# Performance work log

Hardware: AMD Instinct MI355X
Metric: run time of the kernel (lower is better)

The kernel has to match this reference:

```python
import jax, jax.numpy as jnp
import numpy as np

NEG_INF = -1e30
D_MODEL = 128


def setup_inputs() -> dict:
    key = jax.random.key(0)
    k1, k2, k3 = jax.random.split(key, 3)
    B, D, Lc, Lq = 64, D_MODEL, 1024, 256
    C = jax.random.normal(k1, (B, D, Lc), dtype=jnp.float32)
    Q = jax.random.normal(k2, (B, D, Lq), dtype=jnp.float32)
    cmask = jnp.ones((B, Lc), dtype=jnp.float32)
    qmask = jnp.ones((B, Lq), dtype=jnp.float32)
    lim = (1.0 / D) ** 0.5
    w = jax.random.uniform(k3, (3 * D,), dtype=jnp.float32, minval=-lim, maxval=lim)
    return {"C": C, "Q": Q, "cmask": cmask, "qmask": qmask, "w": w}


def reference(C, Q, cmask, qmask, w):
    # C: (B, D, Lc), Q: (B, D, Lq), w: (3D,)
    D = C.shape[1]
    Ct = jnp.swapaxes(C, 1, 2)  # (B, Lc, D)
    Qt = jnp.swapaxes(Q, 1, 2)  # (B, Lq, D)
    w1, w2, w3 = w[:D], w[D:2 * D], w[2 * D:]
    # Decomposed trilinear similarity: equivalent to cat([Ct,Qt,Ct*Qt]) @ w
    S = (jnp.einsum('bld,d->bl', Ct, w1)[:, :, None]
         + jnp.einsum('bmd,d->bm', Qt, w2)[:, None, :]
         + jnp.einsum('bld,bmd->blm', Ct * w3, Qt))  # (B, Lc, Lq)
    qm = qmask[:, None, :]  # (B, 1, Lq)
    cm = cmask[:, :, None]  # (B, Lc, 1)
    S1 = jax.nn.softmax(S + (1.0 - qm) * NEG_INF, axis=2)
    S2 = jax.nn.softmax(S + (1.0 - cm) * NEG_INF, axis=1)
    A = jnp.einsum('blm,bmd->bld', S1, Qt)  # (B, Lc, D)
    S12 = jnp.einsum('blm,bnm->bln', S1, S2)  # (B, Lc, Lc)
    Bv = jnp.einsum('bln,bnd->bld', S12, Ct)  # (B, Lc, D)
    out = jnp.concatenate([Ct, A, Ct * A, Ct * Bv], axis=2)  # (B, Lc, 4D)
    # dropout is identity in eval mode
    return jnp.swapaxes(out, 1, 2)  # (B, 4D, Lc)
```

## Files before the change

### kernel.cpp

```cpp
#include <hip/hip_runtime.h>

#define NB  64
#define ND  128
#define NLC 1024
#define NLQ 256
#define FNEG (-1e30f)

typedef __bf16 bf16x8 __attribute__((ext_vector_type(8)));
typedef float f32x4 __attribute__((ext_vector_type(4)));

__device__ __forceinline__ ushort f2bf(float x) {
  unsigned u = __float_as_uint(x);
  return (ushort)((u + 0x7fffu + ((u >> 16) & 1u)) >> 16);
}
__device__ __forceinline__ float bf2f(ushort u) {
  return __uint_as_float((unsigned)u << 16);
}
__device__ __forceinline__ bf16x8 ldfrag(const ushort* p) {
  return *reinterpret_cast<const bf16x8*>(p);
}
__device__ __forceinline__ uint4 pack8(float a0, float a1, float a2, float a3,
                                       float a4, float a5, float a6, float a7) {
  uint4 pk;
  pk.x = (unsigned)f2bf(a0) | ((unsigned)f2bf(a1) << 16);
  pk.y = (unsigned)f2bf(a2) | ((unsigned)f2bf(a3) << 16);
  pk.z = (unsigned)f2bf(a4) | ((unsigned)f2bf(a5) << 16);
  pk.w = (unsigned)f2bf(a6) | ((unsigned)f2bf(a7) << 16);
  return pk;
}
__device__ __forceinline__ void gl_lds16(const ushort* g, ushort* l) {
  __builtin_amdgcn_global_load_lds(
      (const __attribute__((address_space(1))) unsigned int*)g,
      (__attribute__((address_space(3))) unsigned int*)l, 16, 0, 0);
}

__global__ __launch_bounds__(256) void convert_kernel(
    const float* __restrict__ C, const float* __restrict__ Q,
    const float* __restrict__ w,
    ushort* __restrict__ Ctw3, ushort* __restrict__ Qt16,
    ushort* __restrict__ Cn16, ushort* __restrict__ Qn16,
    float* __restrict__ c1part, float* __restrict__ q2part,
    float* __restrict__ out) {
  __shared__ float tile[64][65];
  __shared__ float cred[64][4];
  int b = blockIdx.y;
  int tid = blockIdx.x;
  int t = threadIdx.x, c = t & 63, r0 = t >> 6;
  if (tid < 32) {
    int d0 = (tid >> 4) * 64, l0 = (tid & 15) * 64;
    const float* src = C + (size_t)b * ND * NLC;
    float* o0 = out + (size_t)b * 4 * ND * NLC;
    ushort* cn = Cn16 + (size_t)b * ND * NLC;
    float part = 0.f;
#pragma unroll
    for (int p = 0; p < 16; ++p) {
      int r = r0 + p * 4;
      size_t idx = (size_t)(d0 + r) * NLC + l0 + c;
      float v = src[idx];
      tile[c][r] = v * w[2 * ND + d0 + r];
      part += v * w[d0 + r];
      o0[idx] = v;
      cn[idx] = f2bf(v);
    }
    cred[c][r0] = part;
    __syncthreads();
    ushort* dst = Ctw3 + (size_t)b * NLC * ND;
#pragma unroll
    for (int p = 0; p < 16; ++p) {
      int r = r0 + p * 4;
      dst[(size_t)(l0 + r) * ND + d0 + c] = f2bf(tile[r][c]);
    }
    if (t < 64)
      c1part[(size_t)(tid >> 4) * NB * NLC + b * NLC + l0 + t] =
          cred[t][0] + cred[t][1] + cred[t][2] + cred[t][3];
  } else {
    int q = tid - 32;
    int d0 = (q >> 2) * 64, m0 = (q & 3) * 64;
    const float* src = Q + (size_t)b * ND * NLQ;
    ushort* qn = Qn16 + (size_t)b * ND * NLQ;
    float part = 0.f;
#pragma unroll
    for (int p = 0; p < 16; ++p) {
      int r = r0 + p * 4;
      size_t idx = (size_t)(d0 + r) * NLQ + m0 + c;
      float v = src[idx];
      tile[c][r] = v;
      part += v * w[ND + d0 + r];
      qn[idx] = f2bf(v);
    }
    cred[c][r0] = part;
    __syncthreads();
    ushort* dst = Qt16 + (size_t)b * NLQ * ND;
#pragma unroll
    for (int p = 0; p < 16; ++p) {
      int r = r0 + p * 4;
      dst[(size_t)(m0 + r) * ND + d0 + c] = f2bf(tile[r][c]);
    }
    if (t < 64)
      q2part[(size_t)(q >> 2) * NB * NLQ + b * NLQ + m0 + t] =
          cred[t][0] + cred[t][1] + cred[t][2] + cred[t][3];
  }
}

__global__ __launch_bounds__(512, 4) void score_stats(
    const ushort* __restrict__ Ctw3, const ushort* __restrict__ Qt16,
    const float* __restrict__ c1part, const float* __restrict__ q2part,
    const float* __restrict__ cmask, const float* __restrict__ qmask,
    ushort* __restrict__ e1g, ushort* __restrict__ e1t,
    float* __restrict__ psum_part, float* __restrict__ chunkmax_g) {
  __shared__ union {
    struct { __align__(16) ushort As[128 * 32]; __align__(16) ushort Bs[256 * 32]; } s;
    struct { float rowred[128][4]; float rowsum[128][4]; float colred[256][2]; } red;
    __align__(16) ushort bounce[128 * 264];
    __align__(16) ushort bounce2[256 * 136];
  } u;
  __shared__ float rmaxs[128];
  __shared__ float rcs[128];
  __shared__ float rss[128];
  __shared__ float cnegs[128];
  __shared__ float qnegs[256];
  __shared__ float c1s[128];
  __shared__ float q2s[256];
  __shared__ float chunkmax_s;

  int b = blockIdx.y, chunk = blockIdx.x, l0 = chunk * 128;
  int t = threadIdx.x, lane = t & 63, wid = t >> 6;
  int wy = wid >> 2, wx = wid & 3, ln = lane & 15, qd = lane >> 4;

  if (t < 128) {
    int idx = b * NLC + l0 + t;
    c1s[t] = c1part[idx] + c1part[NB * NLC + idx];
    cnegs[t] = (1.f - cmask[idx]) * FNEG;
  } else if (t < 384) {
    int m = t - 128;
    int idx = b * NLQ + m;
    q2s[m] = q2part[idx] + q2part[NB * NLQ + idx];
    qnegs[m] = (1.f - qmask[idx]) * FNEG;
  }

  const ushort* Ab = Ctw3 + (size_t)b * NLC * ND;
  const ushort* Bb = Qt16 + (size_t)b * NLQ * ND;
  f32x4 acc[4][4];
#pragma unroll
  for (int i = 0; i < 4; ++i)
#pragma unroll
    for (int j = 0; j < 4; ++j) acc[i][j] = (f32x4){0.f, 0.f, 0.f, 0.f};

  for (int kk = 0; kk < ND; kk += 32) {
#pragma unroll
    for (int p = 0; p < 3; ++p) {
      int e4 = p * 512 + t;
      if (e4 < 512) {
        int r = e4 >> 2, cc = (e4 & 3) * 8;
        gl_lds16(Ab + (size_t)(l0 + r) * ND + kk + cc, u.s.As + e4 * 8);
      } else {
        int e = e4 - 512;
        int r = e >> 2, cc = (e & 3) * 8;
        gl_lds16(Bb + (size_t)r * ND + kk + cc, u.s.Bs + e * 8);
      }
    }
    __syncthreads();
    bf16x8 af[4], bfr[4];
#pragma unroll
    for (int i = 0; i < 4; ++i) {
      af[i]  = ldfrag(u.s.As + (wy * 64 + i * 16 + ln) * 32 + qd * 8);
      bfr[i] = ldfrag(u.s.Bs + (wx * 64 + i * 16 + ln) * 32 + qd * 8);
    }
#pragma unroll
    for (int i = 0; i < 4; ++i)
#pragma unroll
      for (int j = 0; j < 4; ++j)
        acc[i][j] = __builtin_amdgcn_mfma_f32_16x16x32_bf16(af[i], bfr[j], acc[i][j], 0, 0, 0);
    __syncthreads();
  }

  float qnj[4], q2j[4];
#pragma unroll
  for (int j = 0; j < 4; ++j) {
    int m = wx * 64 + j * 16 + ln;
    qnj[j] = qnegs[m];
    q2j[j] = q2s[m];
  }
#pragma unroll
  for (int i = 0; i < 4; ++i)
#pragma unroll
    for (int r = 0; r < 4; ++r) {
      int ll = wy * 64 + i * 16 + qd * 4 + r;
      float cv = c1s[ll];
#pragma unroll
      for (int j = 0; j < 4; ++j) acc[i][j][r] += cv + q2j[j];
    }

#pragma unroll
  for (int i = 0; i < 4; ++i)
#pragma unroll
    for (int r = 0; r < 4; ++r) {
      float v = -INFINITY;
#pragma unroll
      for (int j = 0; j < 4; ++j) v = fmaxf(v, acc[i][j][r] + qnj[j]);
      v = fmaxf(v, __shfl_xor(v, 1));
      v = fmaxf(v, __shfl_xor(v, 2));
      v = fmaxf(v, __shfl_xor(v, 4));
      v = fmaxf(v, __shfl_xor(v, 8));
      if (ln == 0) u.red.rowred[wy * 64 + i * 16 + qd * 4 + r][wx] = v;
    }
  __syncthreads();
  if (t < 128) {
    float v = fmaxf(fmaxf(u.red.rowred[t][0], u.red.rowred[t][1]),
                    fmaxf(u.red.rowred[t][2], u.red.rowred[t][3]));
    rmaxs[t] = v;
    rcs[t] = v + cnegs[t];
  }
  __syncthreads();
  if (t < 64) {
    float v = fmaxf(rcs[t], rcs[t + 64]);
    v = fmaxf(v, __shfl_xor(v, 1));
    v = fmaxf(v, __shfl_xor(v, 2));
    v = fmaxf(v, __shfl_xor(v, 4));
    v = fmaxf(v, __shfl_xor(v, 8));
    v = fmaxf(v, __shfl_xor(v, 16));
    v = fmaxf(v, __shfl_xor(v, 32));
    if (t == 0) chunkmax_s = v;
  }
  __syncthreads();
  if (t < 128) rcs[t] = __expf(rcs[t] - chunkmax_s);
  __syncthreads();

  float cs[4] = {0.f, 0.f, 0.f, 0.f};
#pragma unroll
  for (int i = 0; i < 4; ++i)
#pragma unroll
    for (int r = 0; r < 4; ++r) {
      int ll = wy * 64 + i * 16 + qd * 4 + r;
      float rmx = rmaxs[ll], rf = rcs[ll];
      float rs = 0.f;
#pragma unroll
      for (int j = 0; j < 4; ++j) {
        float e = __expf(acc[i][j][r] + qnj[j] - rmx);
        acc[i][j][r] = e;
        rs += e;
        cs[j] += e * rf;
      }
      rs += __shfl_xor(rs, 1);
      rs += __shfl_xor(rs, 2);
      rs += __shfl_xor(rs, 4);
      rs += __shfl_xor(rs, 8);
      if (ln == 0) u.red.rowsum[ll][wx] = rs;
    }
#pragma unroll
  for (int j = 0; j < 4; ++j) {
    float v = cs[j];
    v += __shfl_xor(v, 16);
    v += __shfl_xor(v, 32);
    if (qd == 0) u.red.colred[wx * 64 + j * 16 + ln][wy] = v;
  }
  __syncthreads();
  if (t < 128)
    rss[t] = 1.f / (u.red.rowsum[t][0] + u.red.rowsum[t][1] +
                    u.red.rowsum[t][2] + u.red.rowsum[t][3]);
  if (t >= 256 && t < 512) {
    int m = t - 256;
    psum_part[(b * 8 + chunk) * NLQ + m] = u.red.colred[m][0] + u.red.colred[m][1];
  }
  if (t == 0) chunkmax_g[b * 8 + chunk] = chunkmax_s;
  __syncthreads();

#pragma unroll
  for (int i = 0; i < 4; ++i)
#pragma unroll
    for (int r = 0; r < 4; ++r) {
      int ll = wy * 64 + i * 16 + qd * 4 + r;
      float rs = rss[ll];
#pragma unroll
      for (int j = 0; j < 4; ++j)
        u.bounce[ll * 264 + wx * 64 + j * 16 + ln] = f2bf(acc[i][j][r] * rs);
    }
  __syncthreads();
  ushort* Eb = e1g + (size_t)b * NLC * NLQ;
#pragma unroll
  for (int p = 0; p < 8; ++p) {
    int idx4 = p * 512 + t;
    int r = idx4 >> 5, c = (idx4 & 31) * 8;
    *(int4*)(Eb + (size_t)(l0 + r) * NLQ + c) = *(const int4*)(u.bounce + r * 264 + c);
  }
  __syncthreads();

#pragma unroll
  for (int i = 0; i < 4; ++i)
#pragma unroll
    for (int r = 0; r < 4; ++r) {
      int ll = wy * 64 + i * 16 + qd * 4 + r;
      float rf = rcs[ll];
#pragma unroll
      for (int j = 0; j < 4; ++j)
        u.bounce2[(wx * 64 + j * 16 + ln) * 136 + ll] = f2bf(acc[i][j][r] * rf);
    }
  __syncthreads();
  ushort* Etb = e1t + (size_t)b * NLQ * NLC;
#pragma unroll
  for (int p = 0; p < 8; ++p) {
    int idx4 = p * 512 + t;
    int m = idx4 >> 4, l8 = idx4 & 15;
    *(int4*)(Etb + (size_t)m * NLC + l0 + l8 * 8) =
        *(const int4*)(u.bounce2 + m * 136 + l8 * 8);
  }
}

__global__ __launch_bounds__(256) void stat_combine(
    const float* __restrict__ psum_part, const float* __restrict__ chunkmax_g,
    float* __restrict__ cinv) {
  __shared__ float cm[8];
  int b = blockIdx.x, t = threadIdx.x;
  if (t < 8) cm[t] = chunkmax_g[b * 8 + t];
  __syncthreads();
  float K = cm[0];
#pragma unroll
  for (int c = 1; c < 8; ++c) K = fmaxf(K, cm[c]);
  float s = 0.f;
#pragma unroll
  for (int c = 0; c < 8; ++c)
    s += psum_part[(b * 8 + c) * NLQ + t] * __expf(cm[c] - K);
  cinv[b * NLQ + t] = 1.f / s;
}

__global__ __launch_bounds__(256, 2) void tmat_mfma(
    const ushort* __restrict__ Cn16, const ushort* __restrict__ e1t,
    const float* __restrict__ chunkmax_g, ushort* __restrict__ Tpart) {
  __shared__ __align__(16) ushort As[128 * 32];
  __shared__ __align__(16) ushort Bs[128 * 32];
  int b = blockIdx.y, ksm = blockIdx.x, ks = ksm >> 1, mh = ksm & 1;
  int t = threadIdx.x, lane = t & 63, wid = t >> 6;
  int wy = wid >> 1, wx = wid & 1, ln = lane & 15, qd = lane >> 4;
  const ushort* Cb = Cn16 + (size_t)b * ND * NLC;
  const ushort* Eb = e1t + (size_t)b * NLQ * NLC + (size_t)(mh * 128) * NLC;
  float cm0 = chunkmax_g[b * 8 + 2 * ks];
  float cm1 = chunkmax_g[b * 8 + 2 * ks + 1];
  int first = (cm0 <= cm1) ? 0 : 1;
  float resc = __expf(fminf(cm0, cm1) - fmaxf(cm0, cm1));
  f32x4 acc[4][4];
#pragma unroll
  for (int i = 0; i < 4; ++i)
#pragma unroll
    for (int j = 0; j < 4; ++j) acc[i][j] = (f32x4){0.f, 0.f, 0.f, 0.f};

  for (int h = 0; h < 2; ++h) {
    int lbase = (2 * ks + (h ? 1 - first : first)) * 128;
    for (int c0 = 0; c0 < 128; c0 += 32) {
#pragma unroll
      for (int p = 0; p < 2; ++p) {
        int e4 = p * 256 + t;
        int r = e4 >> 2, cc = (e4 & 3) * 8;
        gl_lds16(Cb + (size_t)r * NLC + lbase + c0 + cc, As + e4 * 8);
        gl_lds16(Eb + (size_t)r * NLC + lbase + c0 + cc, Bs + e4 * 8);
      }
      __syncthreads();
      bf16x8 af[4], bfr[4];
#pragma unroll
      for (int i = 0; i < 4; ++i) {
        af[i]  = ldfrag(As + (wy * 64 + i * 16 + ln) * 32 + qd * 8);
        bfr[i] = ldfrag(Bs + (wx * 64 + i * 16 + ln) * 32 + qd * 8);
      }
#pragma unroll
      for (int i = 0; i < 4; ++i)
#pragma unroll
        for (int j = 0; j < 4; ++j)
          acc[i][j] = __builtin_amdgcn_mfma_f32_16x16x32_bf16(af[i], bfr[j], acc[i][j], 0, 0, 0);
      __syncthreads();
    }
    if (h == 0) {
#pragma unroll
      for (int i = 0; i < 4; ++i)
#pragma unroll
        for (int j = 0; j < 4; ++j)
#pragma unroll
          for (int r = 0; r < 4; ++r) acc[i][j][r] *= resc;
    }
  }
  ushort* Tb = Tpart + ((size_t)(b * 4 + ks)) * ND * NLQ;
#pragma unroll
  for (int i = 0; i < 4; ++i)
#pragma unroll
    for (int r = 0; r < 4; ++r) {
      int d = wy * 64 + i * 16 + qd * 4 + r;
#pragma unroll
      for (int j = 0; j < 4; ++j) {
        int m = mh * 128 + wx * 64 + j * 16 + ln;
        Tb[(size_t)d * NLQ + m] = f2bf(acc[i][j][r]);
      }
    }
}

__global__ __launch_bounds__(256) void tcombine(
    const ushort* __restrict__ Tpart, const float* __restrict__ cinv,
    const float* __restrict__ chunkmax_g, ushort* __restrict__ Tt) {
  int gid = blockIdx.x * 256 + threadIdx.x;
  int e = gid * 8;
  int b = e >> 15;
  int r = e & 32767;
  int m = r & 255;
  const float* cmb = chunkmax_g + b * 8;
  float K = cmb[0];
#pragma unroll
  for (int c = 1; c < 8; ++c) K = fmaxf(K, cmb[c]);
  float s[8] = {0.f, 0.f, 0.f, 0.f, 0.f, 0.f, 0.f, 0.f};
#pragma unroll
  for (int ks = 0; ks < 4; ++ks) {
    float fac = __expf(fmaxf(cmb[2 * ks], cmb[2 * ks + 1]) - K);
    int4 v = *(const int4*)(Tpart + ((size_t)(b * 4 + ks)) * ND * NLQ + r);
    const ushort* sv = (const ushort*)&v;
#pragma unroll
    for (int k = 0; k < 8; ++k) s[k] += fac * bf2f(sv[k]);
  }
  float4 ci0 = *(const float4*)(cinv + b * NLQ + m);
  float4 ci1 = *(const float4*)(cinv + b * NLQ + m + 4);
  *(uint4*)(Tt + (size_t)b * ND * NLQ + r) =
      pack8(s[0] * ci0.x, s[1] * ci0.y, s[2] * ci0.z, s[3] * ci0.w,
            s[4] * ci1.x, s[5] * ci1.y, s[6] * ci1.z, s[7] * ci1.w);
}

__global__ __launch_bounds__(512, 4) void outk(
    const float* __restrict__ C, const ushort* __restrict__ Qn16,
    const ushort* __restrict__ Tt, const ushort* __restrict__ e1g,
    float* __restrict__ out) {
  __shared__ union {
    struct { __align__(16) ushort As1[128 * 32]; __align__(16) ushort As2[128 * 32];
             __align__(16) ushort Bs[128 * 32]; } st;
    struct { float a[32][132]; float bv[32][132]; } ep;
  } u;
  int b = blockIdx.y;
  int l0 = blockIdx.x * 128;
  const ushort* Qb = Qn16 + (size_t)b * ND * NLQ;
  const ushort* Tb = Tt + (size_t)b * ND * NLQ;
  const ushort* Eb = e1g + (size_t)b * NLC * NLQ;
  int t = threadIdx.x, lane = t & 63, wid = t >> 6;
  int wy = wid >> 2, wx = wid & 3;
  int ln = lane & 15, qd = lane >> 4;
  f32x4 acc1[4][2], acc2[4][2];
#pragma unroll
  for (int i = 0; i < 4; ++i)
#pragma unroll
    for (int j = 0; j < 2; ++j) {
      acc1[i][j] = (f32x4){0.f, 0.f, 0.f, 0.f};
      acc2[i][j] = (f32x4){0.f, 0.f, 0.f, 0.f};
    }

  for (int m0 = 0; m0 < NLQ; m0 += 32) {
    {
      int r = t >> 2, cc = (t & 3) * 8;
      gl_lds16(Qb + (size_t)r * NLQ + m0 + cc, u.st.As1 + t * 8);
      gl_lds16(Tb + (size_t)r * NLQ + m0 + cc, u.st.As2 + t * 8);
      gl_lds16(Eb + (size_t)(l0 + r) * NLQ + m0 + cc, u.st.Bs + t * 8);
    }
    __syncthreads();
    bf16x8 a1[4], a2[4], bfr[2];
#pragma unroll
    for (int i = 0; i < 4; ++i) {
      a1[i] = ldfrag(u.st.As1 + (wy * 64 + i * 16 + ln) * 32 + qd * 8);
      a2[i] = ldfrag(u.st.As2 + (wy * 64 + i * 16 + ln) * 32 + qd * 8);
    }
#pragma unroll
    for (int j = 0; j < 2; ++j)
      bfr[j] = ldfrag(u.st.Bs + (wx * 32 + j * 16 + ln) * 32 + qd * 8);
#pragma unroll
    for (int i = 0; i < 4; ++i)
#pragma unroll
      for (int j = 0; j < 2; ++j) {
        acc1[i][j] = __builtin_amdgcn_mfma_f32_16x16x32_bf16(a1[i], bfr[j], acc1[i][j], 0, 0, 0);
        acc2[i][j] = __builtin_amdgcn_mfma_f32_16x16x32_bf16(a2[i], bfr[j], acc2[i][j], 0, 0, 0);
      }
    __syncthreads();
  }

  const float* Cbase = C + (size_t)b * ND * NLC;
  float* outb = out + (size_t)b * 4 * ND * NLC;
#pragma unroll
  for (int db = 0; db < 4; ++db) {
    __syncthreads();
    if (wy == (db >> 1)) {
      int ibase = (db & 1) * 2;
#pragma unroll
      for (int ii = 0; ii < 2; ++ii) {
        int i = ibase + ii;
#pragma unroll
        for (int j = 0; j < 2; ++j) {
          int lc = wx * 32 + j * 16 + ln;
#pragma unroll
          for (int r = 0; r < 4; ++r) {
            int dr = ii * 16 + qd * 4 + r;
            u.ep.a[dr][lc]  = acc1[i][j][r];
            u.ep.bv[dr][lc] = acc2[i][j][r];
          }
        }
      }
    }
    __syncthreads();
    int row = t >> 4, colf = (t & 15) * 8;
    int d = db * 32 + row;
    const float* Crow = Cbase + (size_t)d * NLC + l0 + colf;
    float4 c0 = *(const float4*)(Crow), c1 = *(const float4*)(Crow + 4);
    float4 a0 = *(const float4*)&u.ep.a[row][colf];
    float4 a1v = *(const float4*)&u.ep.a[row][colf + 4];
    float4 b0 = *(const float4*)&u.ep.bv[row][colf];
    float4 b1 = *(const float4*)&u.ep.bv[row][colf + 4];
    float* oA = outb + (size_t)(128 + d) * NLC + l0 + colf;
    float* oCA = outb + (size_t)(256 + d) * NLC + l0 + colf;
    float* oCB = outb + (size_t)(384 + d) * NLC + l0 + colf;
    *(float4*)(oA) = a0;
    *(float4*)(oA + 4) = a1v;
    *(float4*)(oCA) = (float4){c0.x * a0.x, c0.y * a0.y, c0.z * a0.z, c0.w * a0.w};
    *(float4*)(oCA + 4) = (float4){c1.x * a1v.x, c1.y * a1v.y, c1.z * a1v.z, c1.w * a1v.w};
    *(float4*)(oCB) = (float4){c0.x * b0.x, c0.y * b0.y, c0.z * b0.z, c0.w * b0.w};
    *(float4*)(oCB + 4) = (float4){c1.x * b1.x, c1.y * b1.y, c1.z * b1.z, c1.w * b1.w};
  }
}

extern "C" void kernel_launch(void* const* d_in, const int* in_sizes, int n_in,
                              void* d_out, int out_size, void* d_ws, size_t ws_size,
                              hipStream_t stream) {
  const float* C     = (const float*)d_in[0];
  const float* Q     = (const float*)d_in[1];
  const float* cmask = (const float*)d_in[2];
  const float* qmask = (const float*)d_in[3];
  const float* w     = (const float*)d_in[4];
  float* out = (float*)d_out;

  char* p = (char*)d_ws;
  auto alloc = [&](size_t bytes) { char* r = p; p += (bytes + 255) & ~(size_t)255; return r; };
  ushort* e1g    = (ushort*)alloc((size_t)NB * NLC * NLQ * 2);
  ushort* e1t    = (ushort*)alloc((size_t)NB * NLQ * NLC * 2);
  ushort* Ctw3   = (ushort*)alloc((size_t)NB * NLC * ND * 2);
  ushort* Qt16   = (ushort*)alloc((size_t)NB * NLQ * ND * 2);
  ushort* Cn16   = (ushort*)alloc((size_t)NB * ND * NLC * 2);
  ushort* Qn16   = (ushort*)alloc((size_t)NB * ND * NLQ * 2);
  ushort* Tpart  = (ushort*)alloc((size_t)NB * 4 * ND * NLQ * 2);
  ushort* Tt     = (ushort*)alloc((size_t)NB * ND * NLQ * 2);
  float*  c1part = (float*)alloc((size_t)2 * NB * NLC * 4);
  float*  q2part = (float*)alloc((size_t)2 * NB * NLQ * 4);
  float*  cinv   = (float*)alloc((size_t)NB * NLQ * 4);
  float*  psum   = (float*)alloc((size_t)NB * 8 * NLQ * 4);
  float*  chmax  = (float*)alloc((size_t)NB * 8 * 4);

  convert_kernel<<<dim3(40, NB), 256, 0, stream>>>(C, Q, w, Ctw3, Qt16, Cn16, Qn16,
                                                   c1part, q2part, out);
  score_stats<<<dim3(NLC / 128, NB), 512, 0, stream>>>(
      Ctw3, Qt16, c1part, q2part, cmask, qmask, e1g, e1t, psum, chmax);
  stat_combine<<<NB, 256, 0, stream>>>(psum, chmax, cinv);
  tmat_mfma<<<dim3(8, NB), 256, 0, stream>>>(Cn16, e1t, chmax, Tpart);
  tcombine<<<(NB * ND * NLQ / 8) / 256, 256, 0, stream>>>(Tpart, cinv, chmax, Tt);
  outk<<<dim3(NLC / 128, NB), 512, 0, stream>>>(C, Qn16, Tt, e1g, out);
}
```

Measured before the change: 275.6 us.

## Fuse stat_combine and tcombine into outk; swap async LDS loads in score_stats

The two small combine kernels are removed. outk now computes the column softmax normaliser and the chunk rescale factors itself, and sums the four Tpart slices while staging its A2 tile into shared memory. This drops two launches and the Tt/cinv round trip through global memory. In exchange, each of the 8 outk blocks per batch repeats the combine work and reads four partial tiles instead of one. Separately, score_stats replaces its direct global-to-LDS loads with ordinary register loads followed by LDS stores.

```diff
diff --git a/kernel.cpp b/kernel.cpp
--- a/kernel.cpp
+++ b/kernel.cpp
@@ -152,11 +152,11 @@
       int e4 = p * 512 + t;
       if (e4 < 512) {
         int r = e4 >> 2, cc = (e4 & 3) * 8;
-        gl_lds16(Ab + (size_t)(l0 + r) * ND + kk + cc, u.s.As + e4 * 8);
+        *(int4*)(u.s.As + r * 32 + cc) = *(const int4*)(Ab + (size_t)(l0 + r) * ND + kk + cc);
       } else {
         int e = e4 - 512;
         int r = e >> 2, cc = (e & 3) * 8;
-        gl_lds16(Bb + (size_t)r * ND + kk + cc, u.s.Bs + e * 8);
+        *(int4*)(u.s.Bs + r * 32 + cc) = *(const int4*)(Bb + (size_t)r * ND + kk + cc);
       }
     }
     __syncthreads();
@@ -304,23 +304,6 @@
     *(int4*)(Etb + (size_t)m * NLC + l0 + l8 * 8) =
         *(const int4*)(u.bounce2 + m * 136 + l8 * 8);
   }
-}
-
-__global__ __launch_bounds__(256) void stat_combine(
-    const float* __restrict__ psum_part, const float* __restrict__ chunkmax_g,
-    float* __restrict__ cinv) {
-  __shared__ float cm[8];
-  int b = blockIdx.x, t = threadIdx.x;
-  if (t < 8) cm[t] = chunkmax_g[b * 8 + t];
-  __syncthreads();
-  float K = cm[0];
-#pragma unroll
-  for (int c = 1; c < 8; ++c) K = fmaxf(K, cm[c]);
-  float s = 0.f;
-#pragma unroll
-  for (int c = 0; c < 8; ++c)
-    s += psum_part[(b * 8 + c) * NLQ + t] * __expf(cm[c] - K);
-  cinv[b * NLQ + t] = 1.f / s;
 }
 
 __global__ __launch_bounds__(256, 2) void tmat_mfma(
@@ -390,51 +373,46 @@
     }
 }
 
-__global__ __launch_bounds__(256) void tcombine(
-    const ushort* __restrict__ Tpart, const float* __restrict__ cinv,
-    const float* __restrict__ chunkmax_g, ushort* __restrict__ Tt) {
-  int gid = blockIdx.x * 256 + threadIdx.x;
-  int e = gid * 8;
-  int b = e >> 15;
-  int r = e & 32767;
-  int m = r & 255;
-  const float* cmb = chunkmax_g + b * 8;
-  float K = cmb[0];
-#pragma unroll
-  for (int c = 1; c < 8; ++c) K = fmaxf(K, cmb[c]);
-  float s[8] = {0.f, 0.f, 0.f, 0.f, 0.f, 0.f, 0.f, 0.f};
-#pragma unroll
-  for (int ks = 0; ks < 4; ++ks) {
-    float fac = __expf(fmaxf(cmb[2 * ks], cmb[2 * ks + 1]) - K);
-    int4 v = *(const int4*)(Tpart + ((size_t)(b * 4 + ks)) * ND * NLQ + r);
-    const ushort* sv = (const ushort*)&v;
-#pragma unroll
-    for (int k = 0; k < 8; ++k) s[k] += fac * bf2f(sv[k]);
-  }
-  float4 ci0 = *(const float4*)(cinv + b * NLQ + m);
-  float4 ci1 = *(const float4*)(cinv + b * NLQ + m + 4);
-  *(uint4*)(Tt + (size_t)b * ND * NLQ + r) =
-      pack8(s[0] * ci0.x, s[1] * ci0.y, s[2] * ci0.z, s[3] * ci0.w,
-            s[4] * ci1.x, s[5] * ci1.y, s[6] * ci1.z, s[7] * ci1.w);
-}
-
 __global__ __launch_bounds__(512, 4) void outk(
     const float* __restrict__ C, const ushort* __restrict__ Qn16,
-    const ushort* __restrict__ Tt, const ushort* __restrict__ e1g,
+    const ushort* __restrict__ Tpart, const ushort* __restrict__ e1g,
+    const float* __restrict__ psum_part, const float* __restrict__ chunkmax_g,
     float* __restrict__ out) {
   __shared__ union {
     struct { __align__(16) ushort As1[128 * 32]; __align__(16) ushort As2[128 * 32];
              __align__(16) ushort Bs[128 * 32]; } st;
     struct { float a[32][132]; float bv[32][132]; } ep;
   } u;
+  __shared__ float cinv_s[256];
   int b = blockIdx.y;
   int l0 = blockIdx.x * 128;
   const ushort* Qb = Qn16 + (size_t)b * ND * NLQ;
-  const ushort* Tb = Tt + (size_t)b * ND * NLQ;
+  const ushort* Tp = Tpart + (size_t)(b * 4) * ND * NLQ;
   const ushort* Eb = e1g + (size_t)b * NLC * NLQ;
   int t = threadIdx.x, lane = t & 63, wid = t >> 6;
   int wy = wid >> 2, wx = wid & 3;
   int ln = lane & 15, qd = lane >> 4;
+
+  const float* cmb = chunkmax_g + b * 8;
+  float cmv[8];
+#pragma unroll
+  for (int c = 0; c < 8; ++c) cmv[c] = cmb[c];
+  float K = cmv[0];
+#pragma unroll
+  for (int c = 1; c < 8; ++c) K = fmaxf(K, cmv[c]);
+  float fac[4];
+#pragma unroll
+  for (int ks = 0; ks < 4; ++ks)
+    fac[ks] = __expf(fmaxf(cmv[2 * ks], cmv[2 * ks + 1]) - K);
+  if (t < 256) {
+    float s = 0.f;
+#pragma unroll
+    for (int c = 0; c < 8; ++c)
+      s += psum_part[(b * 8 + c) * NLQ + t] * __expf(cmv[c] - K);
+    cinv_s[t] = 1.f / s;
+  }
+  __syncthreads();
+
   f32x4 acc1[4][2], acc2[4][2];
 #pragma unroll
   for (int i = 0; i < 4; ++i)
@@ -448,8 +426,21 @@
     {
       int r = t >> 2, cc = (t & 3) * 8;
       gl_lds16(Qb + (size_t)r * NLQ + m0 + cc, u.st.As1 + t * 8);
-      gl_lds16(Tb + (size_t)r * NLQ + m0 + cc, u.st.As2 + t * 8);
       gl_lds16(Eb + (size_t)(l0 + r) * NLQ + m0 + cc, u.st.Bs + t * 8);
+      float s[8] = {0.f, 0.f, 0.f, 0.f, 0.f, 0.f, 0.f, 0.f};
+#pragma unroll
+      for (int ks = 0; ks < 4; ++ks) {
+        int4 v = *(const int4*)(Tp + (size_t)ks * ND * NLQ + (size_t)r * NLQ + m0 + cc);
+        const ushort* sv = (const ushort*)&v;
+#pragma unroll
+        for (int k = 0; k < 8; ++k) s[k] += fac[ks] * bf2f(sv[k]);
+      }
+      float ci[8];
+#pragma unroll
+      for (int k = 0; k < 8; ++k) ci[k] = cinv_s[m0 + cc + k];
+      *(uint4*)(u.st.As2 + t * 8) =
+          pack8(s[0] * ci[0], s[1] * ci[1], s[2] * ci[2], s[3] * ci[3],
+                s[4] * ci[4], s[5] * ci[5], s[6] * ci[6], s[7] * ci[7]);
     }
     __syncthreads();
     bf16x8 a1[4], a2[4], bfr[2];
@@ -533,10 +524,8 @@
   ushort* Cn16   = (ushort*)alloc((size_t)NB * ND * NLC * 2);
   ushort* Qn16   = (ushort*)alloc((size_t)NB * ND * NLQ * 2);
   ushort* Tpart  = (ushort*)alloc((size_t)NB * 4 * ND * NLQ * 2);
-  ushort* Tt     = (ushort*)alloc((size_t)NB * ND * NLQ * 2);
   float*  c1part = (float*)alloc((size_t)2 * NB * NLC * 4);
   float*  q2part = (float*)alloc((size_t)2 * NB * NLQ * 4);
-  float*  cinv   = (float*)alloc((size_t)NB * NLQ * 4);
   float*  psum   = (float*)alloc((size_t)NB * 8 * NLQ * 4);
   float*  chmax  = (float*)alloc((size_t)NB * 8 * 4);
 
@@ -544,8 +533,6 @@
                                                    c1part, q2part, out);
   score_stats<<<dim3(NLC / 128, NB), 512, 0, stream>>>(
       Ctw3, Qt16, c1part, q2part, cmask, qmask, e1g, e1t, psum, chmax);
-  stat_combine<<<NB, 256, 0, stream>>>(psum, chmax, cinv);
   tmat_mfma<<<dim3(8, NB), 256, 0, stream>>>(Cn16, e1t, chmax, Tpart);
-  tcombine<<<(NB * ND * NLQ / 8) / 256, 256, 0, stream>>>(Tpart, cinv, chmax, Tt);
-  outk<<<dim3(NLC / 128, NB), 512, 0, stream>>>(C, Qn16, Tt, e1g, out);
-}
+  outk<<<dim3(NLC / 128, NB), 512, 0, stream>>>(C, Qn16, Tpart, e1g, psum, chmax, out);
+}
```

Result: slower. 305.6 us (+10.9%).
